# Performance work log

Hardware: AMD Instinct MI355X
Metric: run time of the kernel (lower is better)

Reference implementation:

```python
import jax, jax.numpy as jnp
import numpy as np

N_NODES = 100000
N_EDGES = 1600000
IN_FEATS = 64
HIDDEN = 32
OUT_FEATS = 40


def _linear_init(key, fan_in, fan_out):
    kw, kb = jax.random.split(key)
    bound = 1.0 / np.sqrt(fan_in)
    W = jax.random.uniform(kw, (fan_in, fan_out), jnp.float32, -bound, bound)
    b = jax.random.uniform(kb, (fan_out,), jnp.float32, -bound, bound)
    return W, b


def setup_inputs() -> dict:
    key = jax.random.key(0)
    ks = jax.random.split(key, 8)
    x = jax.random.normal(ks[0], (N_NODES, IN_FEATS), jnp.float32)
    edge_index = jax.random.randint(ks[1], (2, N_EDGES), 0, N_NODES, jnp.int64)
    W_self1, b_self1 = _linear_init(ks[2], IN_FEATS, HIDDEN)
    W_neigh1, b_neigh1 = _linear_init(ks[3], IN_FEATS, HIDDEN)
    W_self2, b_self2 = _linear_init(ks[4], HIDDEN, HIDDEN)
    W_neigh2, b_neigh2 = _linear_init(ks[5], HIDDEN, HIDDEN)
    W_out, b_out = _linear_init(ks[6], HIDDEN, OUT_FEATS)
    W_lin1, b_lin1 = _linear_init(ks[7], IN_FEATS, OUT_FEATS)
    return {"x": x, "edge_index": edge_index,
            "W_self1": W_self1, "b_self1": b_self1,
            "W_neigh1": W_neigh1, "b_neigh1": b_neigh1,
            "W_self2": W_self2, "b_self2": b_self2,
            "W_neigh2": W_neigh2, "b_neigh2": b_neigh2,
            "W_out": W_out, "b_out": b_out,
            "W_lin1": W_lin1, "b_lin1": b_lin1}


def _scatter_mean(feats, src, dst, num_nodes):
    # gather neighbor features [E, F], sum into destinations, divide by degree
    msgs = feats[src]
    agg = jax.ops.segment_sum(msgs, dst, num_segments=num_nodes)
    cnt = jax.ops.segment_sum(jnp.ones((src.shape[0],), feats.dtype), dst,
                              num_segments=num_nodes)
    return agg / jnp.maximum(cnt, 1.0)[:, None]


def _intra_conv(h, src, dst, W_self, b_self, W_neigh, b_neigh, num_nodes):
    # scatter-mean aggregation + fused linear/residual(self)/relu
    x_self = h @ W_self + b_self
    neigh = _scatter_mean(h, src, dst, num_nodes)
    out = neigh @ W_neigh + b_neigh + x_self
    return jax.nn.relu(out)


def reference(x, edge_index, W_self1, b_self1, W_neigh1, b_neigh1,
              W_self2, b_self2, W_neigh2, b_neigh2, W_out, b_out,
              W_lin1, b_lin1):
    num_nodes = x.shape[0]
    src, dst = edge_index[0], edge_index[1]  # PyG source_to_target flow
    initial_x = x @ W_lin1 + b_lin1  # computed in original forward (unused in output)
    h = _intra_conv(x, src, dst, W_self1, b_self1, W_neigh1, b_neigh1, num_nodes)
    h = _intra_conv(h, src, dst, W_self2, b_self2, W_neigh2, b_neigh2, num_nodes)
    # hidden dim == 32 so x32 is the last layer's output (== h); dropout is eval no-op
    x32 = h
    logits = h @ W_out + b_out
    return (x32, logits)
```

## Files before the change

### kernel.cpp

```cpp
#include <hip/hip_runtime.h>

#define NN 100000
#define NE 1600000
#define RB 256
#define NPB 391
#define CAP 8192
#define GS 32

typedef unsigned int uint;
typedef unsigned short ushort;
typedef __fp16 fp16x2 __attribute__((ext_vector_type(2)));

__device__ __forceinline__ float blo(uint u){ return __uint_as_float(u << 16); }
__device__ __forceinline__ float bhi(uint u){ return __uint_as_float(u & 0xffff0000u); }
__device__ __forceinline__ float b2f(ushort u){ return __uint_as_float(((uint)u) << 16); }
__device__ __forceinline__ ushort f2b(float f){
  uint u = __float_as_uint(f);
  uint r = (u + 0x7fffu + ((u >> 16) & 1u)) >> 16;
  return (ushort)r;
}
__device__ __forceinline__ uint packh2(float a, float b){
  union { fp16x2 h; uint u; } c; c.h = __builtin_amdgcn_cvt_pkrtz(a, b); return c.u;
}
__device__ __forceinline__ float h2lo(uint u){
  union { uint u; fp16x2 h; } c; c.u = u; return (float)c.h.x;
}
__device__ __forceinline__ float h2hi(uint u){
  union { uint u; fp16x2 h; } c; c.u = u; return (float)c.h.y;
}
__device__ __forceinline__ float ldf(const void* p, int i, bool isb){
  return isb ? b2f(((const ushort*)p)[i]) : ((const float*)p)[i];
}

__global__ void prep_k(const uint* __restrict__ xw,  const int* __restrict__ ei,
                       const void* __restrict__ Ws1, const void* __restrict__ bs1,
                       const void* __restrict__ Wn1, const void* __restrict__ bn1,
                       const void* __restrict__ Ws2, const void* __restrict__ bs2,
                       const void* __restrict__ Wn2, const void* __restrict__ bn2,
                       const void* __restrict__ Wo,  const void* __restrict__ bo,
                       float* __restrict__ wc1, float* __restrict__ bc1,
                       float* __restrict__ wc2, float* __restrict__ bc2,
                       float* __restrict__ wof, float* __restrict__ bof,
                       float* __restrict__ bn1f, float* __restrict__ bn2f,
                       int* __restrict__ flags, int* __restrict__ gcur)
{
  int t = threadIdx.x;
  __shared__ int nz, bcnt;
  __shared__ int s_isb;
  if (t == 0) { nz = 0; bcnt = 0; }
  __syncthreads();

  int hiw = ei[2 * t + 1];
  if (hiw != 0) atomicOr(&nz, 1);

  uint u = xw[t];
  uint le = (u >> 7) & 0xFFu;
  if (le == 0u || (le >= 96u && le <= 144u)) atomicAdd(&bcnt, 1);
  __syncthreads();
  if (t == 0) s_isb = (bcnt >= 240) ? 1 : 0;
  if (blockIdx.x == 0 && t == 0) {
    flags[0] = (bcnt >= 240) ? 1 : 0;
    flags[1] = (nz == 0) ? 1 : 0;
  }
  __syncthreads();
  bool isb = (s_isb != 0);

  if (blockIdx.x == 0) gcur[t * GS] = t * CAP;

  int g0 = blockIdx.x * 256 + t, gs = gridDim.x * 256;
  for (int i = g0; i < 64 * 64; i += gs) {
    int f = i >> 6, j = i & 63;
    wc1[i] = (j < 32) ? ldf(Ws1, f * 32 + j, isb) : ldf(Wn1, f * 32 + (j - 32), isb);
  }
  for (int i = g0; i < 64; i += gs) bc1[i] = (i < 32) ? ldf(bs1, i, isb) : 0.f;
  for (int i = g0; i < 32 * 64; i += gs) {
    int f = i >> 6, j = i & 63;
    wc2[i] = (j < 32) ? ldf(Ws2, f * 32 + j, isb) : ldf(Wn2, f * 32 + (j - 32), isb);
  }
  for (int i = g0; i < 64; i += gs) bc2[i] = (i < 32) ? ldf(bs2, i, isb) : 0.f;
  for (int i = g0; i < 32 * 40; i += gs) wof[i] = ldf(Wo, i, isb);
  for (int i = g0; i < 40; i += gs) bof[i] = ldf(bo, i, isb);
  for (int i = g0; i < 32; i += gs) bn1f[i] = ldf(bn1, i, isb);
  for (int i = g0; i < 32; i += gs) bn2f[i] = ldf(bn2, i, isb);
}

__device__ __forceinline__ void part_body(const int* __restrict__ ei,
                                          const int* __restrict__ flags,
                                          int2* __restrict__ pairs,
                                          int* __restrict__ gcur, int E, int blk)
{
  __shared__ int hist[RB];
  __shared__ int gbase[RB];
  int m = flags[1];
  int base = blk * 2048;
  hist[threadIdx.x] = 0;
  __syncthreads();
  int bk[8], rk[8]; int2 prs[8];
#pragma unroll
  for (int k = 0; k < 8; k++) {
    int e = base + threadIdx.x + k * 256;
    bk[k] = -1;
    if (e < E) {
      int dd = m ? ei[2 * (E + e)] : ei[E + e];
      int s  = m ? ei[2 * e] : ei[e];
      bk[k] = dd / NPB;
      rk[k] = atomicAdd(&hist[bk[k]], 1);
      prs[k] = make_int2(dd, s);
    }
  }
  __syncthreads();
  if (hist[threadIdx.x] > 0)
    gbase[threadIdx.x] = atomicAdd(&gcur[threadIdx.x * GS], hist[threadIdx.x]);
  __syncthreads();
#pragma unroll
  for (int k = 0; k < 8; k++) {
    if (bk[k] >= 0) {
      int pos = gbase[bk[k]] + rk[k];
      if (pos < (bk[k] + 1) * CAP) pairs[pos] = prs[k];
    }
  }
}

template <int IN, bool XDYN>
__device__ __forceinline__ void transform_body(const void* __restrict__ xin,
                                               const float* __restrict__ W,
                                               const float* __restrict__ bias,
                                               float* __restrict__ tself,
                                               uint* __restrict__ tneigh,
                                               const int* __restrict__ flags, int n)
{
  bool isb = XDYN ? (flags[0] != 0) : false;
  float xr[IN];
  if (XDYN && isb) {
    const uint4* p = (const uint4*)((const ushort*)xin + (size_t)n * IN);
#pragma unroll
    for (int k = 0; k < IN / 8; k++) {
      uint4 v = p[k];
      xr[8 * k + 0] = blo(v.x); xr[8 * k + 1] = bhi(v.x);
      xr[8 * k + 2] = blo(v.y); xr[8 * k + 3] = bhi(v.y);
      xr[8 * k + 4] = blo(v.z); xr[8 * k + 5] = bhi(v.z);
      xr[8 * k + 6] = blo(v.w); xr[8 * k + 7] = bhi(v.w);
    }
  } else {
    const float4* p = (const float4*)((const float*)xin + (size_t)n * IN);
#pragma unroll
    for (int k = 0; k < IN / 4; k++) {
      float4 v = p[k];
      xr[4 * k + 0] = v.x; xr[4 * k + 1] = v.y; xr[4 * k + 2] = v.z; xr[4 * k + 3] = v.w;
    }
  }
#pragma unroll 1
  for (int j0 = 0; j0 < 64; j0 += 32) {
    float acc[32];
#pragma unroll
    for (int jj = 0; jj < 32; jj++) acc[jj] = bias[j0 + jj];
#pragma unroll 8
    for (int f = 0; f < IN; f++) {
      float xv = xr[f];
#pragma unroll
      for (int jj = 0; jj < 32; jj++)
        acc[jj] = fmaf(xv, W[f * 64 + j0 + jj], acc[jj]);
    }
    if (j0 == 0) {
      float* o = tself + (size_t)n * 32;
#pragma unroll
      for (int q = 0; q < 8; q++)
        ((float4*)o)[q] = make_float4(acc[4 * q], acc[4 * q + 1], acc[4 * q + 2], acc[4 * q + 3]);
    } else {
      uint* o = tneigh + (size_t)n * 16;
#pragma unroll
      for (int q = 0; q < 4; q++) {
        uint4 v;
        v.x = packh2(acc[8 * q + 0], acc[8 * q + 1]);
        v.y = packh2(acc[8 * q + 2], acc[8 * q + 3]);
        v.z = packh2(acc[8 * q + 4], acc[8 * q + 5]);
        v.w = packh2(acc[8 * q + 6], acc[8 * q + 7]);
        ((uint4*)o)[q] = v;
      }
    }
  }
}

__global__ __launch_bounds__(256) void part_t1_k(const int* __restrict__ ei,
                                                 const int* __restrict__ flags,
                                                 int2* __restrict__ pairs,
                                                 int* __restrict__ gcur, int E,
                                                 const void* __restrict__ x,
                                                 const float* __restrict__ wc1,
                                                 const float* __restrict__ bc1,
                                                 float* __restrict__ tself,
                                                 uint* __restrict__ tneigh,
                                                 int N, int PB)
{
  if ((int)blockIdx.x < PB) {
    part_body(ei, flags, pairs, gcur, E, (int)blockIdx.x);
  } else {
    int n = ((int)blockIdx.x - PB) * 256 + threadIdx.x;
    if (n < N) transform_body<64, true>(x, wc1, bc1, tself, tneigh, flags, n);
  }
}

__global__ __launch_bounds__(512) void csr_bucket_k(const int2* __restrict__ pairs,
                                                    const int* __restrict__ gcur,
                                                    int2* __restrict__ desc,
                                                    int* __restrict__ col)
{
  __shared__ int lh[NPB];
  __shared__ int ps[512];
  __shared__ int cs[RB];
  int t = threadIdx.x;
  int r = blockIdx.x;
  if (t < RB) cs[t] = min(gcur[t * GS] - t * CAP, CAP);
  __syncthreads();
  if (t < RB) ps[t] = cs[t];
  __syncthreads();
  for (int off = 1; off < RB; off <<= 1) {
    int v = (t < RB && t >= off) ? ps[t - off] : 0;
    __syncthreads();
    if (t < RB) ps[t] += v;
    __syncthreads();
  }
  int n    = cs[r];
  int base = ps[r] - n;
  __syncthreads();

  int lo = r * NPB;
  int nn = min(NPB, NN - lo);
  int b0 = r * CAP;
  for (int j = t; j < NPB; j += 512) lh[j] = 0;
  __syncthreads();
  for (int i = b0 + t; i < b0 + n; i += 512)
    atomicAdd(&lh[pairs[i].x - lo], 1);
  __syncthreads();
  int v = (t < nn) ? lh[t] : 0;
  ps[t] = v;
  __syncthreads();
  for (int off = 1; off < 512; off <<= 1) {
    int x = (t >= off) ? ps[t - off] : 0;
    __syncthreads();
    ps[t] += x;
    __syncthreads();
  }
  int excl = base + ps[t] - v;
  if (t < nn) desc[lo + t] = make_int2(excl, v);
  __syncthreads();
  if (t < nn) lh[t] = excl;
  __syncthreads();
  for (int i = b0 + t; i < b0 + n; i += 512) {
    int2 pr = pairs[i];
    int p = atomicAdd(&lh[pr.x - lo], 1);
    col[p] = pr.y;
  }
}

__device__ __forceinline__ void agg_core(const float* __restrict__ tself,
                                         const uint* __restrict__ tneigh,
                                         const int2* __restrict__ desc,
                                         const int* __restrict__ col,
                                         const float* __restrict__ bneigh,
                                         int d, int lane,
                                         float& v0, float& v1, float& v2, float& v3)
{
  int slot = lane >> 3, f4 = lane & 7;
  int2 dd = desc[d];
  int start = dd.x, deg = dd.y, end = start + deg;
  float a0 = 0.f, a1 = 0.f, a2 = 0.f, a3 = 0.f;
  for (int base = start; base < end; base += 64) {
    int cnt = min(64, end - base);
    int ce = (lane < cnt) ? col[base + lane] : 0;
#pragma unroll 1
    for (int j = 0; j < cnt; j += 16) {
      int k0 = j + slot, k1 = j + 8 + slot;
      int i0 = __shfl(ce, k0, 64);
      int i1 = __shfl(ce, k1, 64);
      uint2 u0 = make_uint2(0, 0), u1 = make_uint2(0, 0);
      if (k0 < cnt) u0 = ((const uint2*)(tneigh + (size_t)i0 * 16))[f4];
      if (k1 < cnt) u1 = ((const uint2*)(tneigh + (size_t)i1 * 16))[f4];
      a0 += h2lo(u0.x) + h2lo(u1.x);
      a1 += h2hi(u0.x) + h2hi(u1.x);
      a2 += h2lo(u0.y) + h2lo(u1.y);
      a3 += h2hi(u0.y) + h2hi(u1.y);
    }
  }
  a0 += __shfl_xor(a0, 8, 64);  a1 += __shfl_xor(a1, 8, 64);
  a2 += __shfl_xor(a2, 8, 64);  a3 += __shfl_xor(a3, 8, 64);
  a0 += __shfl_xor(a0, 16, 64); a1 += __shfl_xor(a1, 16, 64);
  a2 += __shfl_xor(a2, 16, 64); a3 += __shfl_xor(a3, 16, 64);
  a0 += __shfl_xor(a0, 32, 64); a1 += __shfl_xor(a1, 32, 64);
  a2 += __shfl_xor(a2, 32, 64); a3 += __shfl_xor(a3, 32, 64);
  float scale = 1.0f / (float)max(deg, 1);
  float4 self = ((const float4*)(tself + (size_t)d * 32))[f4];
  float4 bn   = ((const float4*)bneigh)[f4];
  v0 = fmaxf(fmaf(a0, scale, bn.x + self.x), 0.f);
  v1 = fmaxf(fmaf(a1, scale, bn.y + self.y), 0.f);
  v2 = fmaxf(fmaf(a2, scale, bn.z + self.z), 0.f);
  v3 = fmaxf(fmaf(a3, scale, bn.w + self.w), 0.f);
}

__device__ __forceinline__ float hfeat(int f, float v0, float v1, float v2, float v3)
{
  int src = f >> 2;
  switch (f & 3) {
    case 0:  return __shfl(v0, src, 64);
    case 1:  return __shfl(v1, src, 64);
    case 2:  return __shfl(v2, src, 64);
    default: return __shfl(v3, src, 64);
  }
}

__global__ __launch_bounds__(256) void agg_t2_k(const float* __restrict__ tself1,
                                                const uint* __restrict__ tneigh1,
                                                const int2* __restrict__ desc,
                                                const int* __restrict__ col,
                                                const float* __restrict__ bn1f,
                                                const float* __restrict__ wc2,
                                                const float* __restrict__ bc2,
                                                float* __restrict__ tself2,
                                                uint* __restrict__ tneigh2)
{
  int w = threadIdx.x >> 6;
  int d = blockIdx.x * 4 + w;
  int lane = threadIdx.x & 63;
  float v0, v1, v2, v3;
  agg_core(tself1, tneigh1, desc, col, bn1f, d, lane, v0, v1, v2, v3);
  float acc = bc2[lane];
#pragma unroll
  for (int f = 0; f < 32; f++)
    acc = fmaf(hfeat(f, v0, v1, v2, v3), wc2[f * 64 + lane], acc);
  if (lane < 32)
    tself2[(size_t)d * 32 + lane] = acc;
  float pl = __shfl(acc, 32 + 2 * (lane & 15), 64);
  float ph = __shfl(acc, 33 + 2 * (lane & 15), 64);
  if (lane < 16)
    tneigh2[(size_t)d * 16 + lane] = packh2(pl, ph);
}

__global__ __launch_bounds__(256) void agg_out_k(const float* __restrict__ tself2,
                                                 const uint* __restrict__ tneigh2,
                                                 const int2* __restrict__ desc,
                                                 const int* __restrict__ col,
                                                 const float* __restrict__ bn2f,
                                                 const float* __restrict__ wof,
                                                 const float* __restrict__ bof,
                                                 void* __restrict__ out,
                                                 const int* __restrict__ flags)
{
  int w = threadIdx.x >> 6;
  int d = blockIdx.x * 4 + w;
  int lane = threadIdx.x & 63;
  float v0, v1, v2, v3;
  agg_core(tself2, tneigh2, desc, col, bn2f, d, lane, v0, v1, v2, v3);
  bool isb = (flags[0] != 0);
  if (lane < 8) {
    if (isb) {
      uint2 pk;
      pk.x = (uint)f2b(v0) | ((uint)f2b(v1) << 16);
      pk.y = (uint)f2b(v2) | ((uint)f2b(v3) << 16);
      ((uint2*)out)[(size_t)d * 8 + lane] = pk;
    } else {
      ((float4*)out)[(size_t)d * 8 + lane] = make_float4(v0, v1, v2, v3);
    }
  }
  int lj = (lane < 40) ? lane : 39;
  float acc = bof[lj];
#pragma unroll
  for (int f = 0; f < 32; f++)
    acc = fmaf(hfeat(f, v0, v1, v2, v3), wof[f * 40 + lj], acc);
  if (isb) {
    float lo = __shfl(acc, 2 * lane, 64);
    float hi = __shfl(acc, 2 * lane + 1, 64);
    if (lane < 20)
      ((uint*)out)[(size_t)NN * 16 + (size_t)d * 20 + lane] =
          (uint)f2b(lo) | ((uint)f2b(hi) << 16);
  } else {
    if (lane < 40)
      ((float*)out)[(size_t)NN * 32 + (size_t)d * 40 + lane] = acc;
  }
}

extern "C" void kernel_launch(void* const* d_in, const int* in_sizes, int n_in,
                              void* d_out, int out_size, void* d_ws, size_t ws_size,
                              hipStream_t stream)
{
  const int N = NN, E = NE;
  const void* x   = d_in[0];
  const int*  ei  = (const int*)d_in[1];

  char* p = (char*)d_ws;
  auto alloc = [&](size_t bytes) -> void* {
    void* r = (void*)p;
    p += (bytes + 255) & ~(size_t)255;
    return r;
  };
  float* wc1  = (float*)alloc(64 * 64 * 4);
  float* bc1  = (float*)alloc(64 * 4);
  float* wc2  = (float*)alloc(32 * 64 * 4);
  float* bc2  = (float*)alloc(64 * 4);
  float* wof  = (float*)alloc(32 * 40 * 4);
  float* bof  = (float*)alloc(40 * 4);
  float* bn1f = (float*)alloc(32 * 4);
  float* bn2f = (float*)alloc(32 * 4);
  int*   flags = (int*)alloc(8);
  int*   gcur = (int*)alloc(RB * GS * 4);
  int2*  desc = (int2*)alloc((size_t)N * 8);
  int*   col  = (int*)alloc((size_t)E * 4);
  int2*  pairs = (int2*)alloc((size_t)RB * CAP * 8);
  float* tself1 = (float*)alloc((size_t)N * 32 * 4);
  uint*  tneigh1 = (uint*)alloc((size_t)N * 16 * 4);
  float* tself2 = (float*)alloc((size_t)N * 32 * 4);
  uint*  tneigh2 = (uint*)pairs;

  const int PB = (E + 2047) / 2048;
  const int TB = (N + 255) / 256;

  prep_k<<<17, 256, 0, stream>>>((const uint*)x, ei,
                                 d_in[2], d_in[3], d_in[4], d_in[5],
                                 d_in[6], d_in[7], d_in[8], d_in[9],
                                 d_in[10], d_in[11],
                                 wc1, bc1, wc2, bc2, wof, bof, bn1f, bn2f,
                                 flags, gcur);
  part_t1_k<<<PB + TB, 256, 0, stream>>>(ei, flags, pairs, gcur, E,
                                         x, wc1, bc1, tself1, tneigh1, N, PB);
  csr_bucket_k<<<RB, 512, 0, stream>>>(pairs, gcur, desc, col);
  agg_t2_k<<<N / 4, 256, 0, stream>>>(tself1, tneigh1, desc, col, bn1f,
                                      wc2, bc2, tself2, tneigh2);
  agg_out_k<<<N / 4, 256, 0, stream>>>(tself2, tneigh2, desc, col, bn2f,
                                       wof, bof, d_out, flags);
}
```

Baseline: 269.3 us.

## Batch neighbor gathers per chunk and use LDS-staged transposed weights for dense layers

The aggregation loop now shuffles all neighbor indices for a 64-edge chunk up front and issues up to eight independent 8-byte gathers before accumulating, so more loads are in flight per wave. The per-node dense projections replace 32 cross-lane shuffles with a small shared-memory staging of the hidden vector plus float4 reads of transposed weight rows prepared in the prep kernel. This adds register pressure from the unrolled gather arrays. The LDS write and read within a wave are not separated by an explicit barrier and depend on wave-synchronous execution.

```diff
diff --git a/kernel.cpp b/kernel.cpp
--- a/kernel.cpp
+++ b/kernel.cpp
@@ -39,8 +39,8 @@
                        const void* __restrict__ Wn2, const void* __restrict__ bn2,
                        const void* __restrict__ Wo,  const void* __restrict__ bo,
                        float* __restrict__ wc1, float* __restrict__ bc1,
-                       float* __restrict__ wc2, float* __restrict__ bc2,
-                       float* __restrict__ wof, float* __restrict__ bof,
+                       float* __restrict__ wc2T, float* __restrict__ bc2,
+                       float* __restrict__ wofT, float* __restrict__ bof,
                        float* __restrict__ bn1f, float* __restrict__ bn2f,
                        int* __restrict__ flags, int* __restrict__ gcur)
 {
@@ -73,12 +73,15 @@
     wc1[i] = (j < 32) ? ldf(Ws1, f * 32 + j, isb) : ldf(Wn1, f * 32 + (j - 32), isb);
   }
   for (int i = g0; i < 64; i += gs) bc1[i] = (i < 32) ? ldf(bs1, i, isb) : 0.f;
-  for (int i = g0; i < 32 * 64; i += gs) {
-    int f = i >> 6, j = i & 63;
-    wc2[i] = (j < 32) ? ldf(Ws2, f * 32 + j, isb) : ldf(Wn2, f * 32 + (j - 32), isb);
+  for (int i = g0; i < 64 * 32; i += gs) {
+    int j = i >> 5, f = i & 31;
+    wc2T[i] = (j < 32) ? ldf(Ws2, f * 32 + j, isb) : ldf(Wn2, f * 32 + (j - 32), isb);
   }
   for (int i = g0; i < 64; i += gs) bc2[i] = (i < 32) ? ldf(bs2, i, isb) : 0.f;
-  for (int i = g0; i < 32 * 40; i += gs) wof[i] = ldf(Wo, i, isb);
+  for (int i = g0; i < 40 * 32; i += gs) {
+    int j = i >> 5, f = i & 31;
+    wofT[i] = ldf(Wo, f * 40 + j, isb);
+  }
   for (int i = g0; i < 40; i += gs) bof[i] = ldf(bo, i, isb);
   for (int i = g0; i < 32; i += gs) bn1f[i] = ldf(bn1, i, isb);
   for (int i = g0; i < 32; i += gs) bn2f[i] = ldf(bn2, i, isb);
@@ -268,18 +271,30 @@
   for (int base = start; base < end; base += 64) {
     int cnt = min(64, end - base);
     int ce = (lane < cnt) ? col[base + lane] : 0;
-#pragma unroll 1
-    for (int j = 0; j < cnt; j += 16) {
-      int k0 = j + slot, k1 = j + 8 + slot;
-      int i0 = __shfl(ce, k0, 64);
-      int i1 = __shfl(ce, k1, 64);
-      uint2 u0 = make_uint2(0, 0), u1 = make_uint2(0, 0);
-      if (k0 < cnt) u0 = ((const uint2*)(tneigh + (size_t)i0 * 16))[f4];
-      if (k1 < cnt) u1 = ((const uint2*)(tneigh + (size_t)i1 * 16))[f4];
-      a0 += h2lo(u0.x) + h2lo(u1.x);
-      a1 += h2hi(u0.x) + h2hi(u1.x);
-      a2 += h2lo(u0.y) + h2lo(u1.y);
-      a3 += h2hi(u0.y) + h2hi(u1.y);
+    int np = (cnt + 7) >> 3;
+    int idx[8];
+#pragma unroll
+    for (int p = 0; p < 8; p++) {
+      idx[p] = 0;
+      if (p < np) idx[p] = __shfl(ce, 8 * p + slot, 64);
+    }
+    uint2 uu[8];
+#pragma unroll
+    for (int p = 0; p < 8; p++) {
+      uu[p] = make_uint2(0u, 0u);
+      if (p < np) {
+        int k = 8 * p + slot;
+        if (k < cnt)
+          uu[p] = *(const uint2*)((const char*)tneigh +
+                                  ((uint)idx[p] * 64u + (uint)f4 * 8u));
+      }
+    }
+#pragma unroll
+    for (int p = 0; p < 8; p++) {
+      if (p < np) {
+        a0 += h2lo(uu[p].x); a1 += h2hi(uu[p].x);
+        a2 += h2lo(uu[p].y); a3 += h2hi(uu[p].y);
+      }
     }
   }
   a0 += __shfl_xor(a0, 8, 64);  a1 += __shfl_xor(a1, 8, 64);
@@ -297,36 +312,36 @@
   v3 = fmaxf(fmaf(a3, scale, bn.w + self.w), 0.f);
 }
 
-__device__ __forceinline__ float hfeat(int f, float v0, float v1, float v2, float v3)
-{
-  int src = f >> 2;
-  switch (f & 3) {
-    case 0:  return __shfl(v0, src, 64);
-    case 1:  return __shfl(v1, src, 64);
-    case 2:  return __shfl(v2, src, 64);
-    default: return __shfl(v3, src, 64);
-  }
-}
-
 __global__ __launch_bounds__(256) void agg_t2_k(const float* __restrict__ tself1,
                                                 const uint* __restrict__ tneigh1,
                                                 const int2* __restrict__ desc,
                                                 const int* __restrict__ col,
                                                 const float* __restrict__ bn1f,
-                                                const float* __restrict__ wc2,
+                                                const float* __restrict__ wc2T,
                                                 const float* __restrict__ bc2,
                                                 float* __restrict__ tself2,
                                                 uint* __restrict__ tneigh2)
 {
-  int w = threadIdx.x >> 6;
+  __shared__ float hsh[4][32];
+  int w = __builtin_amdgcn_readfirstlane(threadIdx.x >> 6);
   int d = blockIdx.x * 4 + w;
   int lane = threadIdx.x & 63;
   float v0, v1, v2, v3;
   agg_core(tself1, tneigh1, desc, col, bn1f, d, lane, v0, v1, v2, v3);
+  if (lane < 8)
+    ((float4*)hsh[w])[lane] = make_float4(v0, v1, v2, v3);
+  const float4* hp = (const float4*)hsh[w];
+  const float4* wp = (const float4*)(wc2T + lane * 32);
   float acc = bc2[lane];
 #pragma unroll
-  for (int f = 0; f < 32; f++)
-    acc = fmaf(hfeat(f, v0, v1, v2, v3), wc2[f * 64 + lane], acc);
+  for (int q = 0; q < 8; q++) {
+    float4 hq = hp[q];
+    float4 wq = wp[q];
+    acc = fmaf(hq.x, wq.x, acc);
+    acc = fmaf(hq.y, wq.y, acc);
+    acc = fmaf(hq.z, wq.z, acc);
+    acc = fmaf(hq.w, wq.w, acc);
+  }
   if (lane < 32)
     tself2[(size_t)d * 32 + lane] = acc;
   float pl = __shfl(acc, 32 + 2 * (lane & 15), 64);
@@ -340,12 +355,13 @@
                                                  const int2* __restrict__ desc,
                                                  const int* __restrict__ col,
                                                  const float* __restrict__ bn2f,
-                                                 const float* __restrict__ wof,
+                                                 const float* __restrict__ wofT,
                                                  const float* __restrict__ bof,
                                                  void* __restrict__ out,
                                                  const int* __restrict__ flags)
 {
-  int w = threadIdx.x >> 6;
+  __shared__ float hsh[4][32];
+  int w = __builtin_amdgcn_readfirstlane(threadIdx.x >> 6);
   int d = blockIdx.x * 4 + w;
   int lane = threadIdx.x & 63;
   float v0, v1, v2, v3;
@@ -360,12 +376,21 @@
     } else {
       ((float4*)out)[(size_t)d * 8 + lane] = make_float4(v0, v1, v2, v3);
     }
+    ((float4*)hsh[w])[lane] = make_float4(v0, v1, v2, v3);
   }
   int lj = (lane < 40) ? lane : 39;
+  const float4* hp = (const float4*)hsh[w];
+  const float4* wp = (const float4*)(wofT + lj * 32);
   float acc = bof[lj];
 #pragma unroll
-  for (int f = 0; f < 32; f++)
-    acc = fmaf(hfeat(f, v0, v1, v2, v3), wof[f * 40 + lj], acc);
+  for (int q = 0; q < 8; q++) {
+    float4 hq = hp[q];
+    float4 wq = wp[q];
+    acc = fmaf(hq.x, wq.x, acc);
+    acc = fmaf(hq.y, wq.y, acc);
+    acc = fmaf(hq.z, wq.z, acc);
+    acc = fmaf(hq.w, wq.w, acc);
+  }
   if (isb) {
     float lo = __shfl(acc, 2 * lane, 64);
     float hi = __shfl(acc, 2 * lane + 1, 64);
@@ -394,9 +419,9 @@
   };
   float* wc1  = (float*)alloc(64 * 64 * 4);
   float* bc1  = (float*)alloc(64 * 4);
-  float* wc2  = (float*)alloc(32 * 64 * 4);
+  float* wc2T = (float*)alloc(64 * 32 * 4);
   float* bc2  = (float*)alloc(64 * 4);
-  float* wof  = (float*)alloc(32 * 40 * 4);
+  float* wofT = (float*)alloc(40 * 32 * 4);
   float* bof  = (float*)alloc(40 * 4);
   float* bn1f = (float*)alloc(32 * 4);
   float* bn2f = (float*)alloc(32 * 4);
@@ -417,13 +442,13 @@
                                  d_in[2], d_in[3], d_in[4], d_in[5],
                                  d_in[6], d_in[7], d_in[8], d_in[9],
                                  d_in[10], d_in[11],
-                                 wc1, bc1, wc2, bc2, wof, bof, bn1f, bn2f,
+                                 wc1, bc1, wc2T, bc2, wofT, bof, bn1f, bn2f,
                                  flags, gcur);
   part_t1_k<<<PB + TB, 256, 0, stream>>>(ei, flags, pairs, gcur, E,
                                          x, wc1, bc1, tself1, tneigh1, N, PB);
   csr_bucket_k<<<RB, 512, 0, stream>>>(pairs, gcur, desc, col);
   agg_t2_k<<<N / 4, 256, 0, stream>>>(tself1, tneigh1, desc, col, bn1f,
-                                      wc2, bc2, tself2, tneigh2);
+                                      wc2T, bc2, tself2, tneigh2);
   agg_out_k<<<N / 4, 256, 0, stream>>>(tself2, tneigh2, desc, col, bn2f,
-                                       wof, bof, d_out, flags);
-}
+                                       wofT, bof, d_out, flags);
+}
```

Result: slower. 347.8 us (+29.2%).

## Replace CSR build and per-node gather with bucketed LDS atomic scatter aggregation

Applied to the files above, without the earlier changes.

Drops the CSR bucket-sort kernel and aggregates straight from the partitioned (dst,src) pair buckets. Each of the 256 blocks (1024 threads) owns a range of 391 destination nodes and accumulates neighbor rows into an LDS accumulator with float atomics, then runs the fused linear/ReLU epilogue per node. This removes one kernel launch and the desc/col construction, and tneigh2 gets its own buffer instead of aliasing pairs. The cost is heavy LDS atomic contention (32 atomics per edge), only 256 blocks of work, and a summation order that is no longer deterministic.

```diff
diff --git a/kernel.cpp b/kernel.cpp
--- a/kernel.cpp
+++ b/kernel.cpp
@@ -200,181 +200,153 @@
   }
 }
 
-__global__ __launch_bounds__(512) void csr_bucket_k(const int2* __restrict__ pairs,
-                                                    const int* __restrict__ gcur,
-                                                    int2* __restrict__ desc,
-                                                    int* __restrict__ col)
-{
-  __shared__ int lh[NPB];
-  __shared__ int ps[512];
-  __shared__ int cs[RB];
+__global__ __launch_bounds__(1024) void agg_l1_k(const int2* __restrict__ pairs,
+                                                 const int* __restrict__ gcur,
+                                                 const float* __restrict__ tself1,
+                                                 const uint* __restrict__ tneigh1,
+                                                 const float* __restrict__ bn1f,
+                                                 const float* __restrict__ wc2,
+                                                 const float* __restrict__ bc2,
+                                                 float* __restrict__ tself2,
+                                                 uint* __restrict__ tneigh2)
+{
+  __shared__ float acc[NPB][33];
+  __shared__ int   deg[NPB];
   int t = threadIdx.x;
   int r = blockIdx.x;
-  if (t < RB) cs[t] = min(gcur[t * GS] - t * CAP, CAP);
-  __syncthreads();
-  if (t < RB) ps[t] = cs[t];
-  __syncthreads();
-  for (int off = 1; off < RB; off <<= 1) {
-    int v = (t < RB && t >= off) ? ps[t - off] : 0;
-    __syncthreads();
-    if (t < RB) ps[t] += v;
-    __syncthreads();
-  }
-  int n    = cs[r];
-  int base = ps[r] - n;
-  __syncthreads();
-
   int lo = r * NPB;
   int nn = min(NPB, NN - lo);
+  for (int i = t; i < NPB * 33; i += 1024) ((float*)acc)[i] = 0.f;
+  for (int i = t; i < NPB; i += 1024) deg[i] = 0;
+  __syncthreads();
+  int cnt = min(gcur[r * GS] - r * CAP, CAP);
   int b0 = r * CAP;
-  for (int j = t; j < NPB; j += 512) lh[j] = 0;
-  __syncthreads();
-  for (int i = b0 + t; i < b0 + n; i += 512)
-    atomicAdd(&lh[pairs[i].x - lo], 1);
-  __syncthreads();
-  int v = (t < nn) ? lh[t] : 0;
-  ps[t] = v;
-  __syncthreads();
-  for (int off = 1; off < 512; off <<= 1) {
-    int x = (t >= off) ? ps[t - off] : 0;
-    __syncthreads();
-    ps[t] += x;
-    __syncthreads();
-  }
-  int excl = base + ps[t] - v;
-  if (t < nn) desc[lo + t] = make_int2(excl, v);
-  __syncthreads();
-  if (t < nn) lh[t] = excl;
-  __syncthreads();
-  for (int i = b0 + t; i < b0 + n; i += 512) {
-    int2 pr = pairs[i];
-    int p = atomicAdd(&lh[pr.x - lo], 1);
-    col[p] = pr.y;
-  }
-}
-
-__device__ __forceinline__ void agg_core(const float* __restrict__ tself,
-                                         const uint* __restrict__ tneigh,
-                                         const int2* __restrict__ desc,
-                                         const int* __restrict__ col,
-                                         const float* __restrict__ bneigh,
-                                         int d, int lane,
-                                         float& v0, float& v1, float& v2, float& v3)
-{
-  int slot = lane >> 3, f4 = lane & 7;
-  int2 dd = desc[d];
-  int start = dd.x, deg = dd.y, end = start + deg;
-  float a0 = 0.f, a1 = 0.f, a2 = 0.f, a3 = 0.f;
-  for (int base = start; base < end; base += 64) {
-    int cnt = min(64, end - base);
-    int ce = (lane < cnt) ? col[base + lane] : 0;
-#pragma unroll 1
-    for (int j = 0; j < cnt; j += 16) {
-      int k0 = j + slot, k1 = j + 8 + slot;
-      int i0 = __shfl(ce, k0, 64);
-      int i1 = __shfl(ce, k1, 64);
-      uint2 u0 = make_uint2(0, 0), u1 = make_uint2(0, 0);
-      if (k0 < cnt) u0 = ((const uint2*)(tneigh + (size_t)i0 * 16))[f4];
-      if (k1 < cnt) u1 = ((const uint2*)(tneigh + (size_t)i1 * 16))[f4];
-      a0 += h2lo(u0.x) + h2lo(u1.x);
-      a1 += h2hi(u0.x) + h2hi(u1.x);
-      a2 += h2lo(u0.y) + h2lo(u1.y);
-      a3 += h2hi(u0.y) + h2hi(u1.y);
-    }
-  }
-  a0 += __shfl_xor(a0, 8, 64);  a1 += __shfl_xor(a1, 8, 64);
-  a2 += __shfl_xor(a2, 8, 64);  a3 += __shfl_xor(a3, 8, 64);
-  a0 += __shfl_xor(a0, 16, 64); a1 += __shfl_xor(a1, 16, 64);
-  a2 += __shfl_xor(a2, 16, 64); a3 += __shfl_xor(a3, 16, 64);
-  a0 += __shfl_xor(a0, 32, 64); a1 += __shfl_xor(a1, 32, 64);
-  a2 += __shfl_xor(a2, 32, 64); a3 += __shfl_xor(a3, 32, 64);
-  float scale = 1.0f / (float)max(deg, 1);
-  float4 self = ((const float4*)(tself + (size_t)d * 32))[f4];
-  float4 bn   = ((const float4*)bneigh)[f4];
-  v0 = fmaxf(fmaf(a0, scale, bn.x + self.x), 0.f);
-  v1 = fmaxf(fmaf(a1, scale, bn.y + self.y), 0.f);
-  v2 = fmaxf(fmaf(a2, scale, bn.z + self.z), 0.f);
-  v3 = fmaxf(fmaf(a3, scale, bn.w + self.w), 0.f);
-}
-
-__device__ __forceinline__ float hfeat(int f, float v0, float v1, float v2, float v3)
-{
-  int src = f >> 2;
-  switch (f & 3) {
-    case 0:  return __shfl(v0, src, 64);
-    case 1:  return __shfl(v1, src, 64);
-    case 2:  return __shfl(v2, src, 64);
-    default: return __shfl(v3, src, 64);
-  }
-}
-
-__global__ __launch_bounds__(256) void agg_t2_k(const float* __restrict__ tself1,
-                                                const uint* __restrict__ tneigh1,
-                                                const int2* __restrict__ desc,
-                                                const int* __restrict__ col,
-                                                const float* __restrict__ bn1f,
-                                                const float* __restrict__ wc2,
-                                                const float* __restrict__ bc2,
-                                                float* __restrict__ tself2,
-                                                uint* __restrict__ tneigh2)
-{
-  int w = threadIdx.x >> 6;
-  int d = blockIdx.x * 4 + w;
-  int lane = threadIdx.x & 63;
-  float v0, v1, v2, v3;
-  agg_core(tself1, tneigh1, desc, col, bn1f, d, lane, v0, v1, v2, v3);
-  float acc = bc2[lane];
-#pragma unroll
-  for (int f = 0; f < 32; f++)
-    acc = fmaf(hfeat(f, v0, v1, v2, v3), wc2[f * 64 + lane], acc);
-  if (lane < 32)
-    tself2[(size_t)d * 32 + lane] = acc;
-  float pl = __shfl(acc, 32 + 2 * (lane & 15), 64);
-  float ph = __shfl(acc, 33 + 2 * (lane & 15), 64);
-  if (lane < 16)
-    tneigh2[(size_t)d * 16 + lane] = packh2(pl, ph);
-}
-
-__global__ __launch_bounds__(256) void agg_out_k(const float* __restrict__ tself2,
+  for (int i = t; i < cnt; i += 1024) {
+    int2 pr = pairs[b0 + i];
+    int n = pr.x - lo;
+    const uint4* row = (const uint4*)(tneigh1 + (size_t)pr.y * 16);
+    uint4 u0 = row[0], u1 = row[1], u2 = row[2], u3 = row[3];
+    atomicAdd(&deg[n], 1);
+    float* an = acc[n];
+    atomicAdd(&an[0],  h2lo(u0.x)); atomicAdd(&an[1],  h2hi(u0.x));
+    atomicAdd(&an[2],  h2lo(u0.y)); atomicAdd(&an[3],  h2hi(u0.y));
+    atomicAdd(&an[4],  h2lo(u0.z)); atomicAdd(&an[5],  h2hi(u0.z));
+    atomicAdd(&an[6],  h2lo(u0.w)); atomicAdd(&an[7],  h2hi(u0.w));
+    atomicAdd(&an[8],  h2lo(u1.x)); atomicAdd(&an[9],  h2hi(u1.x));
+    atomicAdd(&an[10], h2lo(u1.y)); atomicAdd(&an[11], h2hi(u1.y));
+    atomicAdd(&an[12], h2lo(u1.z)); atomicAdd(&an[13], h2hi(u1.z));
+    atomicAdd(&an[14], h2lo(u1.w)); atomicAdd(&an[15], h2hi(u1.w));
+    atomicAdd(&an[16], h2lo(u2.x)); atomicAdd(&an[17], h2hi(u2.x));
+    atomicAdd(&an[18], h2lo(u2.y)); atomicAdd(&an[19], h2hi(u2.y));
+    atomicAdd(&an[20], h2lo(u2.z)); atomicAdd(&an[21], h2hi(u2.z));
+    atomicAdd(&an[22], h2lo(u2.w)); atomicAdd(&an[23], h2hi(u2.w));
+    atomicAdd(&an[24], h2lo(u3.x)); atomicAdd(&an[25], h2hi(u3.x));
+    atomicAdd(&an[26], h2lo(u3.y)); atomicAdd(&an[27], h2hi(u3.y));
+    atomicAdd(&an[28], h2lo(u3.z)); atomicAdd(&an[29], h2hi(u3.z));
+    atomicAdd(&an[30], h2lo(u3.w)); atomicAdd(&an[31], h2hi(u3.w));
+  }
+  __syncthreads();
+  int wv = t >> 6, lane = t & 63, f = lane & 31;
+  for (int n = wv; n < nn; n += 16) {
+    if (lane < 32) {
+      float sc = 1.0f / (float)max(deg[n], 1);
+      float hv = fmaxf(fmaf(acc[n][f], sc,
+                            bn1f[f] + tself1[(size_t)(lo + n) * 32 + f]), 0.f);
+      acc[n][f] = hv;
+    }
+    float aj = bc2[lane];
+#pragma unroll 8
+    for (int f2 = 0; f2 < 32; f2++)
+      aj = fmaf(acc[n][f2], wc2[f2 * 64 + lane], aj);
+    if (lane < 32)
+      tself2[(size_t)(lo + n) * 32 + lane] = aj;
+    float pl = __shfl(aj, 32 + 2 * (lane & 15), 64);
+    float ph = __shfl(aj, 33 + 2 * (lane & 15), 64);
+    if (lane < 16)
+      tneigh2[(size_t)(lo + n) * 16 + lane] = packh2(pl, ph);
+  }
+}
+
+__global__ __launch_bounds__(1024) void agg_l2_k(const int2* __restrict__ pairs,
+                                                 const int* __restrict__ gcur,
+                                                 const float* __restrict__ tself2,
                                                  const uint* __restrict__ tneigh2,
-                                                 const int2* __restrict__ desc,
-                                                 const int* __restrict__ col,
                                                  const float* __restrict__ bn2f,
                                                  const float* __restrict__ wof,
                                                  const float* __restrict__ bof,
                                                  void* __restrict__ out,
                                                  const int* __restrict__ flags)
 {
-  int w = threadIdx.x >> 6;
-  int d = blockIdx.x * 4 + w;
-  int lane = threadIdx.x & 63;
-  float v0, v1, v2, v3;
-  agg_core(tself2, tneigh2, desc, col, bn2f, d, lane, v0, v1, v2, v3);
+  __shared__ float acc[NPB][33];
+  __shared__ int   deg[NPB];
+  int t = threadIdx.x;
+  int r = blockIdx.x;
+  int lo = r * NPB;
+  int nn = min(NPB, NN - lo);
+  for (int i = t; i < NPB * 33; i += 1024) ((float*)acc)[i] = 0.f;
+  for (int i = t; i < NPB; i += 1024) deg[i] = 0;
+  __syncthreads();
+  int cnt = min(gcur[r * GS] - r * CAP, CAP);
+  int b0 = r * CAP;
+  for (int i = t; i < cnt; i += 1024) {
+    int2 pr = pairs[b0 + i];
+    int n = pr.x - lo;
+    const uint4* row = (const uint4*)(tneigh2 + (size_t)pr.y * 16);
+    uint4 u0 = row[0], u1 = row[1], u2 = row[2], u3 = row[3];
+    atomicAdd(&deg[n], 1);
+    float* an = acc[n];
+    atomicAdd(&an[0],  h2lo(u0.x)); atomicAdd(&an[1],  h2hi(u0.x));
+    atomicAdd(&an[2],  h2lo(u0.y)); atomicAdd(&an[3],  h2hi(u0.y));
+    atomicAdd(&an[4],  h2lo(u0.z)); atomicAdd(&an[5],  h2hi(u0.z));
+    atomicAdd(&an[6],  h2lo(u0.w)); atomicAdd(&an[7],  h2hi(u0.w));
+    atomicAdd(&an[8],  h2lo(u1.x)); atomicAdd(&an[9],  h2hi(u1.x));
+    atomicAdd(&an[10], h2lo(u1.y)); atomicAdd(&an[11], h2hi(u1.y));
+    atomicAdd(&an[12], h2lo(u1.z)); atomicAdd(&an[13], h2hi(u1.z));
+    atomicAdd(&an[14], h2lo(u1.w)); atomicAdd(&an[15], h2hi(u1.w));
+    atomicAdd(&an[16], h2lo(u2.x)); atomicAdd(&an[17], h2hi(u2.x));
+    atomicAdd(&an[18], h2lo(u2.y)); atomicAdd(&an[19], h2hi(u2.y));
+    atomicAdd(&an[20], h2lo(u2.z)); atomicAdd(&an[21], h2hi(u2.z));
+    atomicAdd(&an[22], h2lo(u2.w)); atomicAdd(&an[23], h2hi(u2.w));
+    atomicAdd(&an[24], h2lo(u3.x)); atomicAdd(&an[25], h2hi(u3.x));
+    atomicAdd(&an[26], h2lo(u3.y)); atomicAdd(&an[27], h2hi(u3.y));
+    atomicAdd(&an[28], h2lo(u3.z)); atomicAdd(&an[29], h2hi(u3.z));
+    atomicAdd(&an[30], h2lo(u3.w)); atomicAdd(&an[31], h2hi(u3.w));
+  }
+  __syncthreads();
   bool isb = (flags[0] != 0);
-  if (lane < 8) {
+  int wv = t >> 6, lane = t & 63, f = lane & 31;
+  for (int n = wv; n < nn; n += 16) {
+    if (lane < 32) {
+      float sc = 1.0f / (float)max(deg[n], 1);
+      float hv = fmaxf(fmaf(acc[n][f], sc,
+                            bn2f[f] + tself2[(size_t)(lo + n) * 32 + f]), 0.f);
+      acc[n][f] = hv;
+    }
+    size_t d = (size_t)(lo + n);
     if (isb) {
-      uint2 pk;
-      pk.x = (uint)f2b(v0) | ((uint)f2b(v1) << 16);
-      pk.y = (uint)f2b(v2) | ((uint)f2b(v3) << 16);
-      ((uint2*)out)[(size_t)d * 8 + lane] = pk;
+      if (lane < 16) {
+        uint pk = (uint)f2b(acc[n][2 * lane]) |
+                  ((uint)f2b(acc[n][2 * lane + 1]) << 16);
+        ((uint*)out)[d * 16 + lane] = pk;
+      }
     } else {
-      ((float4*)out)[(size_t)d * 8 + lane] = make_float4(v0, v1, v2, v3);
-    }
-  }
-  int lj = (lane < 40) ? lane : 39;
-  float acc = bof[lj];
-#pragma unroll
-  for (int f = 0; f < 32; f++)
-    acc = fmaf(hfeat(f, v0, v1, v2, v3), wof[f * 40 + lj], acc);
-  if (isb) {
-    float lo = __shfl(acc, 2 * lane, 64);
-    float hi = __shfl(acc, 2 * lane + 1, 64);
-    if (lane < 20)
-      ((uint*)out)[(size_t)NN * 16 + (size_t)d * 20 + lane] =
-          (uint)f2b(lo) | ((uint)f2b(hi) << 16);
-  } else {
-    if (lane < 40)
-      ((float*)out)[(size_t)NN * 32 + (size_t)d * 40 + lane] = acc;
+      if (lane < 32) ((float*)out)[d * 32 + lane] = acc[n][lane];
+    }
+    int lj = (lane < 40) ? lane : 39;
+    float aj = bof[lj];
+#pragma unroll 8
+    for (int f2 = 0; f2 < 32; f2++)
+      aj = fmaf(acc[n][f2], wof[f2 * 40 + lj], aj);
+    if (isb) {
+      float lo2 = __shfl(aj, 2 * lane, 64);
+      float hi2 = __shfl(aj, 2 * lane + 1, 64);
+      if (lane < 20)
+        ((uint*)out)[(size_t)NN * 16 + d * 20 + lane] =
+            (uint)f2b(lo2) | ((uint)f2b(hi2) << 16);
+    } else {
+      if (lane < 40)
+        ((float*)out)[(size_t)NN * 32 + d * 40 + lane] = aj;
+    }
   }
 }
 
@@ -402,13 +374,11 @@
   float* bn2f = (float*)alloc(32 * 4);
   int*   flags = (int*)alloc(8);
   int*   gcur = (int*)alloc(RB * GS * 4);
-  int2*  desc = (int2*)alloc((size_t)N * 8);
-  int*   col  = (int*)alloc((size_t)E * 4);
   int2*  pairs = (int2*)alloc((size_t)RB * CAP * 8);
   float* tself1 = (float*)alloc((size_t)N * 32 * 4);
   uint*  tneigh1 = (uint*)alloc((size_t)N * 16 * 4);
   float* tself2 = (float*)alloc((size_t)N * 32 * 4);
-  uint*  tneigh2 = (uint*)pairs;
+  uint*  tneigh2 = (uint*)alloc((size_t)N * 16 * 4);
 
   const int PB = (E + 2047) / 2048;
   const int TB = (N + 255) / 256;
@@ -421,9 +391,8 @@
                                  flags, gcur);
   part_t1_k<<<PB + TB, 256, 0, stream>>>(ei, flags, pairs, gcur, E,
                                          x, wc1, bc1, tself1, tneigh1, N, PB);
-  csr_bucket_k<<<RB, 512, 0, stream>>>(pairs, gcur, desc, col);
-  agg_t2_k<<<N / 4, 256, 0, stream>>>(tself1, tneigh1, desc, col, bn1f,
-                                      wc2, bc2, tself2, tneigh2);
-  agg_out_k<<<N / 4, 256, 0, stream>>>(tself2, tneigh2, desc, col, bn2f,
-                                       wof, bof, d_out, flags);
-}
+  agg_l1_k<<<RB, 1024, 0, stream>>>(pairs, gcur, tself1, tneigh1, bn1f,
+                                    wc2, bc2, tself2, tneigh2);
+  agg_l2_k<<<RB, 1024, 0, stream>>>(pairs, gcur, tself2, tneigh2, bn2f,
+                                    wof, bof, d_out, flags);
+}
```

New measurement: 750.7 us. 2.79x slower.
